# Kernel tuning notes

Measured on AMD Instinct MI355X. Metric: run time of the kernel, lower is better.

## Reference

```python
import jax, jax.numpy as jnp
import numpy as np


def setup_inputs() -> dict:
    key = jax.random.key(0)
    ks = jax.random.split(key, 8)
    N, E, F, H = 50000, 400000, 128, 512
    x = jax.random.normal(ks[0], (N, F), dtype=jnp.float32)
    edge_index = jax.random.randint(ks[1], (2, E), 0, N, dtype=jnp.int32)
    W1 = jax.random.normal(ks[2], (H, 2 * F), dtype=jnp.float32) * 0.05
    b1 = jax.random.normal(ks[3], (H,), dtype=jnp.float32) * 0.05
    W2 = jax.random.normal(ks[4], (H, 2 * H), dtype=jnp.float32) * 0.05
    b2 = jax.random.normal(ks[5], (H,), dtype=jnp.float32) * 0.05
    Wo = jax.random.normal(ks[6], (1, H), dtype=jnp.float32) * 0.05
    bo = jax.random.normal(ks[7], (1,), dtype=jnp.float32) * 0.05
    return {"x": x, "edge_index": edge_index, "W1": W1, "b1": b1,
            "W2": W2, "b2": b2, "Wo": Wo, "bo": bo}


def reference(x, edge_index, W1, b1, W2, b2, Wo, bo):
    # GraphSAGE mean aggregation: agg[dst] = mean over incoming edges of h[src]
    N = x.shape[0]
    src = edge_index[0]
    dst = edge_index[1]
    deg = jax.ops.segment_sum(jnp.ones_like(dst, dtype=x.dtype), dst,
                              num_segments=N)
    inv_deg = 1.0 / jnp.maximum(deg, 1.0)  # clamp_min(1.0)

    def agg_mean(h):
        s = jax.ops.segment_sum(h[src], dst, num_segments=N)  # [N, D]
        return s * inv_deg[:, None]

    # Layer 1: concat(self, neigh) -> Linear -> ReLU (dropout = identity, eval)
    n1 = agg_mean(x)
    h1 = jax.nn.relu(jnp.concatenate([x, n1], axis=1) @ W1.T + b1)
    # Layer 2
    n2 = agg_mean(h1)
    h2 = jax.nn.relu(jnp.concatenate([h1, n2], axis=1) @ W2.T + b2)
    # Output head
    logits = h2 @ Wo.T + bo  # [N, 1]
    return jax.nn.sigmoid(logits)
```

## Files before the change

### kernel.cpp

```cpp
#include <hip/hip_runtime.h>
#include <math.h>


typedef __attribute__((ext_vector_type(8))) short bf16x8;
typedef __attribute__((ext_vector_type(4))) float f32x4;

static inline int ceil_div(int a, int b) { return (a + b - 1) / b; }

__device__ inline float bf2f_lo(unsigned u) { return __builtin_bit_cast(float, u << 16); }
__device__ inline float bf2f_hi(unsigned u) { return __builtin_bit_cast(float, u & 0xffff0000u); }
__device__ inline unsigned f2bf(float f) {
    unsigned u = __builtin_bit_cast(unsigned, f);
    u += 0x7fffu + ((u >> 16) & 1u);
    return u >> 16;
}

#define GLOAD_LDS16(gp, lp)                                                   \
    __builtin_amdgcn_global_load_lds(                                         \
        (__attribute__((address_space(1))) void*)(gp),                        \
        (__attribute__((address_space(3))) void*)(lp), 16, 0, 0)


__global__ void cvt3_hist_kernel(const float* __restrict__ a, unsigned short* __restrict__ ao, int na4,
                                 const float* __restrict__ b, unsigned short* __restrict__ bo, int nb4,
                                 const float* __restrict__ c, unsigned short* __restrict__ co, int nc4,
                                 const int* __restrict__ dst, int* __restrict__ deg, int E,
                                 int cvt_blocks) {
    if ((int)blockIdx.x < cvt_blocks) {
        int i = blockIdx.x * 256 + threadIdx.x;
        const float* in; unsigned short* out; int k;
        if (i < na4)                  { in = a; out = ao; k = i; }
        else if (i < na4 + nb4)       { in = b; out = bo; k = i - na4; }
        else if (i < na4 + nb4 + nc4) { in = c; out = co; k = i - na4 - nb4; }
        else return;
        float4 v = ((const float4*)in)[k];
        ushort4 o;
        o.x = (unsigned short)f2bf(v.x);
        o.y = (unsigned short)f2bf(v.y);
        o.z = (unsigned short)f2bf(v.z);
        o.w = (unsigned short)f2bf(v.w);
        ((ushort4*)out)[k] = o;
    } else {
        int e = (blockIdx.x - cvt_blocks) * 256 + threadIdx.x;
        if (e < E) atomicAdd(&deg[dst[e]], 1);
    }
}


__global__ __launch_bounds__(256) void chunk_reduce(const int* __restrict__ deg,
                                                    int* __restrict__ partial, int N) {
    int base = blockIdx.x * 1024;
    int s = 0;
    for (int i = threadIdx.x; i < 1024; i += 256) {
        int idx = base + i;
        if (idx < N) s += deg[idx];
    }
    #pragma unroll
    for (int off = 32; off; off >>= 1) s += __shfl_down(s, off);
    __shared__ int ws[4];
    if ((threadIdx.x & 63) == 0) ws[threadIdx.x >> 6] = s;
    __syncthreads();
    if (threadIdx.x == 0) partial[blockIdx.x] = ws[0] + ws[1] + ws[2] + ws[3];
}

__global__ void partial_scan(int* __restrict__ partial, int* __restrict__ rowstartN, int P) {
    int lane = threadIdx.x;
    int v = (lane < P) ? partial[lane] : 0;
    int incl = v;
    #pragma unroll
    for (int off = 1; off < 64; off <<= 1) {
        int t = __shfl_up(incl, off);
        if (lane >= off) incl += t;
    }
    if (lane < P) partial[lane] = incl - v;
    if (lane == 63) *rowstartN = incl;
}

__global__ __launch_bounds__(256) void chunk_scan(const int* __restrict__ deg,
                                                  const int* __restrict__ partial,
                                                  int* __restrict__ rowstart,
                                                  int* __restrict__ cursor, int N) {
    int base = blockIdx.x * 1024 + threadIdx.x * 4;
    int v[4];
    #pragma unroll
    for (int j = 0; j < 4; ++j) {
        int i = base + j;
        v[j] = (i < N) ? deg[i] : 0;
    }
    int mysum = v[0] + v[1] + v[2] + v[3];
    int incl = mysum;
    int lane = threadIdx.x & 63, wave = threadIdx.x >> 6;
    #pragma unroll
    for (int off = 1; off < 64; off <<= 1) {
        int t = __shfl_up(incl, off);
        if (lane >= off) incl += t;
    }
    __shared__ int ws[4];
    if (lane == 63) ws[wave] = incl;
    __syncthreads();
    int run = partial[blockIdx.x] + incl - mysum;
    for (int w = 0; w < wave; ++w) run += ws[w];
    #pragma unroll
    for (int j = 0; j < 4; ++j) {
        int i = base + j;
        if (i < N) { rowstart[i] = run; cursor[i] = run; }
        run += v[j];
    }
}

__global__ void bucket_kernel(const int* __restrict__ src, const int* __restrict__ dst,
                              int* __restrict__ cursor, int* __restrict__ ebuf, int E) {
    int e = blockIdx.x * 256 + threadIdx.x;
    if (e < E) {
        int pos = atomicAdd(&cursor[dst[e]], 1);
        ebuf[pos] = src[e];
    }
}


__global__ void gather_mean_128(const int* __restrict__ rowstart, const int* __restrict__ ebuf,
                                const unsigned* __restrict__ featb, unsigned* __restrict__ outb, int N) {
    int w = (blockIdx.x * blockDim.x + threadIdx.x) >> 6;
    int lane = threadIdx.x & 63;
    if (w >= N) return;
    int e0 = rowstart[w], e1 = rowstart[w + 1];
    float ax = 0.0f, ay = 0.0f;
    int i = e0;
    for (; i + 8 <= e1; i += 8) {
        unsigned v0 = featb[(size_t)ebuf[i]     * 64 + lane];
        unsigned v1 = featb[(size_t)ebuf[i + 1] * 64 + lane];
        unsigned v2 = featb[(size_t)ebuf[i + 2] * 64 + lane];
        unsigned v3 = featb[(size_t)ebuf[i + 3] * 64 + lane];
        unsigned v4 = featb[(size_t)ebuf[i + 4] * 64 + lane];
        unsigned v5 = featb[(size_t)ebuf[i + 5] * 64 + lane];
        unsigned v6 = featb[(size_t)ebuf[i + 6] * 64 + lane];
        unsigned v7 = featb[(size_t)ebuf[i + 7] * 64 + lane];
        ax += bf2f_lo(v0) + bf2f_lo(v1) + bf2f_lo(v2) + bf2f_lo(v3)
            + bf2f_lo(v4) + bf2f_lo(v5) + bf2f_lo(v6) + bf2f_lo(v7);
        ay += bf2f_hi(v0) + bf2f_hi(v1) + bf2f_hi(v2) + bf2f_hi(v3)
            + bf2f_hi(v4) + bf2f_hi(v5) + bf2f_hi(v6) + bf2f_hi(v7);
    }
    for (; i < e1; ++i) {
        unsigned v = featb[(size_t)ebuf[i] * 64 + lane];
        ax += bf2f_lo(v); ay += bf2f_hi(v);
    }
    float inv = 1.0f / fmaxf((float)(e1 - e0), 1.0f);
    outb[(size_t)w * 64 + lane] = f2bf(ax * inv) | (f2bf(ay * inv) << 16);
}

__global__ void gather_mean_512(const int* __restrict__ rowstart, const int* __restrict__ ebuf,
                                const unsigned short* __restrict__ featb,
                                unsigned short* __restrict__ outb, int N) {
    int w = (blockIdx.x * blockDim.x + threadIdx.x) >> 6;
    int lane = threadIdx.x & 63;
    if (w >= N) return;
    int e0 = rowstart[w], e1 = rowstart[w + 1];
    float a[8] = {0, 0, 0, 0, 0, 0, 0, 0};
    const uint4* base = (const uint4*)featb;
    int i = e0;
    for (; i + 8 <= e1; i += 8) {
        uint4 v0 = base[(size_t)ebuf[i]     * 64 + lane];
        uint4 v1 = base[(size_t)ebuf[i + 1] * 64 + lane];
        uint4 v2 = base[(size_t)ebuf[i + 2] * 64 + lane];
        uint4 v3 = base[(size_t)ebuf[i + 3] * 64 + lane];
        uint4 v4 = base[(size_t)ebuf[i + 4] * 64 + lane];
        uint4 v5 = base[(size_t)ebuf[i + 5] * 64 + lane];
        uint4 v6 = base[(size_t)ebuf[i + 6] * 64 + lane];
        uint4 v7 = base[(size_t)ebuf[i + 7] * 64 + lane];
        a[0] += bf2f_lo(v0.x) + bf2f_lo(v1.x) + bf2f_lo(v2.x) + bf2f_lo(v3.x)
              + bf2f_lo(v4.x) + bf2f_lo(v5.x) + bf2f_lo(v6.x) + bf2f_lo(v7.x);
        a[1] += bf2f_hi(v0.x) + bf2f_hi(v1.x) + bf2f_hi(v2.x) + bf2f_hi(v3.x)
              + bf2f_hi(v4.x) + bf2f_hi(v5.x) + bf2f_hi(v6.x) + bf2f_hi(v7.x);
        a[2] += bf2f_lo(v0.y) + bf2f_lo(v1.y) + bf2f_lo(v2.y) + bf2f_lo(v3.y)
              + bf2f_lo(v4.y) + bf2f_lo(v5.y) + bf2f_lo(v6.y) + bf2f_lo(v7.y);
        a[3] += bf2f_hi(v0.y) + bf2f_hi(v1.y) + bf2f_hi(v2.y) + bf2f_hi(v3.y)
              + bf2f_hi(v4.y) + bf2f_hi(v5.y) + bf2f_hi(v6.y) + bf2f_hi(v7.y);
        a[4] += bf2f_lo(v0.z) + bf2f_lo(v1.z) + bf2f_lo(v2.z) + bf2f_lo(v3.z)
              + bf2f_lo(v4.z) + bf2f_lo(v5.z) + bf2f_lo(v6.z) + bf2f_lo(v7.z);
        a[5] += bf2f_hi(v0.z) + bf2f_hi(v1.z) + bf2f_hi(v2.z) + bf2f_hi(v3.z)
              + bf2f_hi(v4.z) + bf2f_hi(v5.z) + bf2f_hi(v6.z) + bf2f_hi(v7.z);
        a[6] += bf2f_lo(v0.w) + bf2f_lo(v1.w) + bf2f_lo(v2.w) + bf2f_lo(v3.w)
              + bf2f_lo(v4.w) + bf2f_lo(v5.w) + bf2f_lo(v6.w) + bf2f_lo(v7.w);
        a[7] += bf2f_hi(v0.w) + bf2f_hi(v1.w) + bf2f_hi(v2.w) + bf2f_hi(v3.w)
              + bf2f_hi(v4.w) + bf2f_hi(v5.w) + bf2f_hi(v6.w) + bf2f_hi(v7.w);
    }
    for (; i < e1; ++i) {
        uint4 v = base[(size_t)ebuf[i] * 64 + lane];
        a[0] += bf2f_lo(v.x); a[1] += bf2f_hi(v.x);
        a[2] += bf2f_lo(v.y); a[3] += bf2f_hi(v.y);
        a[4] += bf2f_lo(v.z); a[5] += bf2f_hi(v.z);
        a[6] += bf2f_lo(v.w); a[7] += bf2f_hi(v.w);
    }
    float inv = 1.0f / fmaxf((float)(e1 - e0), 1.0f);
    uint4 o;
    o.x = f2bf(a[0] * inv) | (f2bf(a[1] * inv) << 16);
    o.y = f2bf(a[2] * inv) | (f2bf(a[3] * inv) << 16);
    o.z = f2bf(a[4] * inv) | (f2bf(a[5] * inv) << 16);
    o.w = f2bf(a[6] * inv) | (f2bf(a[7] * inv) << 16);
    ((uint4*)outb)[(size_t)w * 64 + lane] = o;
}

__global__ __launch_bounds__(256) void gemm_mfma(
    const unsigned short* __restrict__ A0,
    const unsigned short* __restrict__ A1,
    const unsigned short* __restrict__ W,
    const float* __restrict__ b,
    unsigned short* __restrict__ outb,
    const float* __restrict__ Wo,
    float* __restrict__ logit,
    int N, int K0, int K1, int C, int mode)
{
    const int nrow = (N + 127) >> 7;
    const int id   = blockIdx.x;
    const int rowb = ((id >> 5) << 3) + (id & 7);
    const int colb = (id >> 3) & 3;
    if (rowb >= nrow) return;

    const int K = K0 + K1;
    const int S = K0;
    __shared__ short As[2][4096];
    __shared__ short Bs[2][4096];

    const int tid  = threadIdx.x;
    const int lane = tid & 63;
    const int wave = tid >> 6;
    const int wm = wave & 1, wn = wave >> 1;
    const int cl = lane & 15, quad = lane >> 4;
    const int row0 = rowb * 128;
    const int col0 = colb * 128;

    const int r = lane >> 2;
    const int j = lane & 3;
    const int trow0 = wave * 32 + r;
    const int trow1 = trow0 + 16;
    const int ar0 = (row0 + trow0 < N) ? row0 + trow0 : N - 1;
    const int ar1 = (row0 + trow1 < N) ? row0 + trow1 : N - 1;
    const size_t aoff0 = (size_t)ar0 * S + j * 8;
    const size_t aoff1 = (size_t)ar1 * S + j * 8;
    const size_t boff0 = (size_t)(col0 + trow0) * K + j * 8;
    const size_t boff1 = (size_t)(col0 + trow1) * K + j * 8;
    const int lds0 = (wave * 32) * 32;
    const int lds1 = (wave * 32 + 16) * 32;

    f32x4 acc[4][4];
    #pragma unroll
    for (int mt = 0; mt < 4; ++mt)
        #pragma unroll
        for (int nt = 0; nt < 4; ++nt)
            acc[mt][nt] = (f32x4){0.f, 0.f, 0.f, 0.f};

    GLOAD_LDS16(A0 + aoff0, &As[0][lds0]);
    GLOAD_LDS16(A0 + aoff1, &As[0][lds1]);
    GLOAD_LDS16(W  + boff0, &Bs[0][lds0]);
    GLOAD_LDS16(W  + boff1, &Bs[0][lds1]);

    const int iters = K >> 5;
    for (int i = 0; i < iters; ++i) {
        const int cur = i & 1;
        __syncthreads();
        if (i + 1 < iters) {
            const int kn = (i + 1) << 5;
            const unsigned short* Ab = (kn < K0) ? (A0 + kn) : (A1 + (kn - K0));
            const unsigned short* Wb = W + kn;
            const int nb = cur ^ 1;
            GLOAD_LDS16(Ab + aoff0, &As[nb][lds0]);
            GLOAD_LDS16(Ab + aoff1, &As[nb][lds1]);
            GLOAD_LDS16(Wb + boff0, &Bs[nb][lds0]);
            GLOAD_LDS16(Wb + boff1, &Bs[nb][lds1]);
        }

        bf16x8 af[4], bfr[4];
        #pragma unroll
        for (int mt = 0; mt < 4; ++mt)
            af[mt] = *(const bf16x8*)&As[cur][(wm * 64 + mt * 16 + cl) * 32 + quad * 8];
        #pragma unroll
        for (int nt = 0; nt < 4; ++nt)
            bfr[nt] = *(const bf16x8*)&Bs[cur][(wn * 64 + nt * 16 + cl) * 32 + quad * 8];

        #pragma unroll
        for (int mt = 0; mt < 4; ++mt)
            #pragma unroll
            for (int nt = 0; nt < 4; ++nt)
                acc[mt][nt] = __builtin_amdgcn_mfma_f32_16x16x32_bf16(
                    af[mt], bfr[nt], acc[mt][nt], 0, 0, 0);
    }

    if (mode == 0) {
        #pragma unroll
        for (int nt = 0; nt < 4; ++nt) {
            const int colx = col0 + wn * 64 + nt * 16 + cl;
            const float bb = b[colx];
            #pragma unroll
            for (int mt = 0; mt < 4; ++mt) {
                #pragma unroll
                for (int rr = 0; rr < 4; ++rr) {
                    int row = row0 + wm * 64 + mt * 16 + quad * 4 + rr;
                    if (row < N)
                        outb[(size_t)row * C + colx] =
                            (unsigned short)f2bf(fmaxf(acc[mt][nt][rr] + bb, 0.0f));
                }
            }
        }
    } else {
        float bv[4], wv2[4];
        #pragma unroll
        for (int nt = 0; nt < 4; ++nt) {
            const int colx = col0 + wn * 64 + nt * 16 + cl;
            bv[nt] = b[colx];
            wv2[nt] = Wo[colx];
        }
        #pragma unroll
        for (int mt = 0; mt < 4; ++mt) {
            #pragma unroll
            for (int rr = 0; rr < 4; ++rr) {
                float s = 0.0f;
                #pragma unroll
                for (int nt = 0; nt < 4; ++nt)
                    s += fmaxf(acc[mt][nt][rr] + bv[nt], 0.0f) * wv2[nt];
                s += __shfl_xor(s, 1);
                s += __shfl_xor(s, 2);
                s += __shfl_xor(s, 4);
                s += __shfl_xor(s, 8);
                int row = row0 + wm * 64 + mt * 16 + quad * 4 + rr;
                if (cl == 0 && row < N) atomicAdd(&logit[row], s);
            }
        }
    }
}

__global__ void head_kernel(const float* __restrict__ logit, const float* __restrict__ bo,
                            float* __restrict__ out, int N) {
    int i = blockIdx.x * 256 + threadIdx.x;
    if (i < N) out[i] = 1.0f / (1.0f + expf(-(logit[i] + bo[0])));
}

extern "C" void kernel_launch(void* const* d_in, const int* in_sizes, int n_in,
                              void* d_out, int out_size, void* d_ws, size_t ws_size,
                              hipStream_t stream) {
    const float* x  = (const float*)d_in[0];
    const int*   ei = (const int*)d_in[1];
    const float* W1 = (const float*)d_in[2];
    const float* b1 = (const float*)d_in[3];
    const float* W2 = (const float*)d_in[4];
    const float* b2 = (const float*)d_in[5];
    const float* Wo = (const float*)d_in[6];
    const float* bo = (const float*)d_in[7];
    float* out = (float*)d_out;

    const int N = in_sizes[0] / 128;
    const int E = in_sizes[1] / 2;
    const int* src = ei;
    const int* dst = ei + E;

    char* ws = (char*)d_ws;
    size_t off = 0;
    auto alloc = [&](size_t bytes) {
        void* p = ws + off;
        off += (bytes + 255) & ~(size_t)255;
        return p;
    };
    int* deg      = (int*)alloc((size_t)N * 4);
    int* rowstart = (int*)alloc((size_t)(N + 1) * 4);
    int* cursor   = (int*)alloc((size_t)N * 4);
    int* partial  = (int*)alloc((size_t)64 * 4);
    int* ebuf     = (int*)alloc((size_t)E * 4);
    float* logit  = (float*)alloc((size_t)N * 4);
    unsigned short* xb  = (unsigned short*)alloc((size_t)N * 128 * 2);
    unsigned short* W1b = (unsigned short*)alloc((size_t)512 * 256 * 2);
    unsigned short* W2b = (unsigned short*)alloc((size_t)512 * 1024 * 2);
    unsigned short* n1b = (unsigned short*)alloc((size_t)N * 128 * 2);
    unsigned short* h1b = (unsigned short*)alloc((size_t)N * 512 * 2);
    unsigned short* n2b = (unsigned short*)alloc((size_t)N * 512 * 2);
    (void)ws_size; (void)n_in; (void)out_size;

    hipMemsetAsync(deg,   0, (size_t)N * 4, stream);
    hipMemsetAsync(logit, 0, (size_t)N * 4, stream);

    const int na4 = N * 128 / 4, nb4 = 512 * 256 / 4, nc4 = 512 * 1024 / 4;
    const int cvt_blocks  = ceil_div(na4 + nb4 + nc4, 256);
    const int hist_blocks = ceil_div(E, 256);
    cvt3_hist_kernel<<<cvt_blocks + hist_blocks, 256, 0, stream>>>(
        x, xb, na4, W1, W1b, nb4, W2, W2b, nc4, dst, deg, E, cvt_blocks);

    const int P = ceil_div(N, 1024);
    chunk_reduce<<<P, 256, 0, stream>>>(deg, partial, N);
    partial_scan<<<1, 64, 0, stream>>>(partial, rowstart + N, P);
    chunk_scan<<<P, 256, 0, stream>>>(deg, partial, rowstart, cursor, N);
    bucket_kernel<<<ceil_div(E, 256), 256, 0, stream>>>(src, dst, cursor, ebuf, E);

    const int nrow = ceil_div(N, 128);
    const int gblocks = ceil_div(nrow, 8) * 8 * 4;

    gather_mean_128<<<ceil_div(N * 64, 256), 256, 0, stream>>>(rowstart, ebuf,
                                                               (const unsigned*)xb, (unsigned*)n1b, N);
    gemm_mfma<<<gblocks, 256, 0, stream>>>(xb, n1b, W1b, b1, h1b, nullptr, nullptr,
                                           N, 128, 128, 512, 0);

    gather_mean_512<<<ceil_div(N * 64, 256), 256, 0, stream>>>(rowstart, ebuf, h1b, n2b, N);
    gemm_mfma<<<gblocks, 256, 0, stream>>>(h1b, n2b, W2b, b2, nullptr, Wo, logit,
                                           N, 512, 512, 512, 1);

    head_kernel<<<ceil_div(N, 256), 256, 0, stream>>>(logit, bo, out, N);
}
```

Before: 351.7 us.

## Deepen GEMM global-to-LDS prefetch to a 4-stage ring with explicit vmcnt wait

The MFMA GEMM previously double-buffered A/B tiles in LDS and waited for all loads at each __syncthreads. It now uses four LDS buffers, keeps two tiles in flight ahead of compute, and replaces the full sync with a partial vmcnt wait plus a raw s_barrier. At the tail it clamps the tile index so loads stay uniform. This aims to hide global load latency better, at the cost of doubled LDS use per block, which may reduce occupancy. It also relies on the hand-encoded waitcnt value being correct for ordering.

```diff
diff --git a/kernel.cpp b/kernel.cpp
--- a/kernel.cpp
+++ b/kernel.cpp
@@ -19,6 +19,8 @@
     __builtin_amdgcn_global_load_lds(                                         \
         (__attribute__((address_space(1))) void*)(gp),                        \
         (__attribute__((address_space(3))) void*)(lp), 16, 0, 0)
+
+#define WAITCNT_VM8 0x0F78
 
 
 __global__ void cvt3_hist_kernel(const float* __restrict__ a, unsigned short* __restrict__ ao, int na4,
@@ -218,8 +220,8 @@
 
     const int K = K0 + K1;
     const int S = K0;
-    __shared__ short As[2][4096];
-    __shared__ short Bs[2][4096];
+    __shared__ short As[4][4096];
+    __shared__ short Bs[4][4096];
 
     const int tid  = threadIdx.x;
     const int lane = tid & 63;
@@ -242,6 +244,18 @@
     const int lds0 = (wave * 32) * 32;
     const int lds1 = (wave * 32 + 16) * 32;
 
+    const int iters = K >> 5;
+
+    auto issue = [&](int t, int s) {
+        const int k0 = t << 5;
+        const unsigned short* Ab = (k0 < K0) ? (A0 + k0) : (A1 + (k0 - K0));
+        const unsigned short* Wb = W + k0;
+        GLOAD_LDS16(Ab + aoff0, &As[s][lds0]);
+        GLOAD_LDS16(Ab + aoff1, &As[s][lds1]);
+        GLOAD_LDS16(Wb + boff0, &Bs[s][lds0]);
+        GLOAD_LDS16(Wb + boff1, &Bs[s][lds1]);
+    };
+
     f32x4 acc[4][4];
     #pragma unroll
     for (int mt = 0; mt < 4; ++mt)
@@ -249,26 +263,17 @@
         for (int nt = 0; nt < 4; ++nt)
             acc[mt][nt] = (f32x4){0.f, 0.f, 0.f, 0.f};
 
-    GLOAD_LDS16(A0 + aoff0, &As[0][lds0]);
-    GLOAD_LDS16(A0 + aoff1, &As[0][lds1]);
-    GLOAD_LDS16(W  + boff0, &Bs[0][lds0]);
-    GLOAD_LDS16(W  + boff1, &Bs[0][lds1]);
-
-    const int iters = K >> 5;
+    issue(0, 0);
+    issue(1, 1);
+
     for (int i = 0; i < iters; ++i) {
-        const int cur = i & 1;
-        __syncthreads();
-        if (i + 1 < iters) {
-            const int kn = (i + 1) << 5;
-            const unsigned short* Ab = (kn < K0) ? (A0 + kn) : (A1 + (kn - K0));
-            const unsigned short* Wb = W + kn;
-            const int nb = cur ^ 1;
-            GLOAD_LDS16(Ab + aoff0, &As[nb][lds0]);
-            GLOAD_LDS16(Ab + aoff1, &As[nb][lds1]);
-            GLOAD_LDS16(Wb + boff0, &Bs[nb][lds0]);
-            GLOAD_LDS16(Wb + boff1, &Bs[nb][lds1]);
-        }
-
+        int t = i + 2;
+        if (t > iters - 1) t = iters - 1;
+        issue(t, (i + 2) & 3);
+        __builtin_amdgcn_s_waitcnt(WAITCNT_VM8);
+        asm volatile("s_barrier" ::: "memory");
+
+        const int cur = i & 3;
         bf16x8 af[4], bfr[4];
         #pragma unroll
         for (int mt = 0; mt < 4; ++mt)
```

Result: slower. 371.7 us (+5.7%).
